# Kernel optimization log

Hardware: AMD Instinct MI355X
Metric: run time of the kernel (lower is better)

Reference implementation:

```python
import jax, jax.numpy as jnp
import numpy as np

N = 8192        # nodes
F_IN = 512      # input feature dim
H1 = 256        # args.hidden1
H2 = 64         # args.hidden2
E = 262144      # edges (avg degree 32)


def setup_inputs() -> dict:
    key = jax.random.key(0)
    ks = jax.random.split(key, 7)
    x = jax.random.normal(ks[0], (N, F_IN), dtype=jnp.float32)
    adj_rows = jax.random.randint(ks[1], (E,), 0, N, dtype=jnp.int32)
    adj_cols = jax.random.randint(ks[2], (E,), 0, N, dtype=jnp.int32)
    adj_vals = jax.random.uniform(ks[3], (E,), dtype=jnp.float32)
    # Xavier-uniform init like reset_parameters()
    def xavier(k, fan_in, fan_out):
        lim = jnp.sqrt(6.0 / (fan_in + fan_out))
        return jax.random.uniform(k, (fan_in, fan_out), jnp.float32, -lim, lim)
    W1 = xavier(ks[4], F_IN, H1)
    W2 = xavier(ks[5], H1, H2)
    W3 = xavier(ks[6], H1, H2)
    return {"x": x, "adj_rows": adj_rows, "adj_cols": adj_cols,
            "adj_vals": adj_vals, "W1": W1, "W2": W2, "W3": W3}


def reference(x, adj_rows, adj_cols, adj_vals, W1, W2, W3):
    n = x.shape[0]

    def spmm(support):
        # sparse [N,N] @ dense [N,D]: gather neighbor rows, scale, scatter-add
        return jax.ops.segment_sum(adj_vals[:, None] * support[adj_cols],
                                   adj_rows, num_segments=n)

    # gc1: dropout(no-op, eval) -> x @ W1 -> SpMM -> relu
    h1 = jax.nn.relu(spmm(x @ W1))
    # gc2 / gc3: identity activation
    mu = spmm(h1 @ W2)
    logvar = spmm(h1 @ W3)
    z = mu  # eval-mode reparameterize returns mu
    # InnerProductDecoder with identity act (dropout no-op in eval)
    adj_recon = z @ z.T  # [N, N]
    return adj_recon, z, mu, logvar
```

## Files before the change

kernel.cpp:

```cpp
#include <hip/hip_runtime.h>
#include <hip/hip_bf16.h>

#define N_NODES 8192
#define F_INDIM 512
#define H1DIM   256
#define H2DIM   64

typedef __bf16 bf16x8 __attribute__((ext_vector_type(8)));
typedef __bf16 bf16x4 __attribute__((ext_vector_type(4)));
typedef __bf16 bf16x2 __attribute__((ext_vector_type(2)));
typedef float  floatx4 __attribute__((ext_vector_type(4)));

__global__ void count_rows(const int* __restrict__ rows, int* __restrict__ cnt, int e) {
    int i = blockIdx.x * blockDim.x + threadIdx.x;
    if (i < e) atomicAdd(&cnt[rows[i]], 1);
}

__global__ void scan_rows(const int* __restrict__ cnt, int* __restrict__ row_ptr,
                          int* __restrict__ cursor, int n) {
    __shared__ int sums[1024];
    int t = threadIdx.x;
    int base = t * 8;
    int loc[8];
    int s = 0;
#pragma unroll
    for (int i = 0; i < 8; ++i) { loc[i] = cnt[base + i]; s += loc[i]; }
    sums[t] = s;
    __syncthreads();
    for (int off = 1; off < 1024; off <<= 1) {
        int v = (t >= off) ? sums[t - off] : 0;
        __syncthreads();
        sums[t] += v;
        __syncthreads();
    }
    int run = sums[t] - s;
#pragma unroll
    for (int i = 0; i < 8; ++i) {
        row_ptr[base + i] = run;
        cursor[base + i]  = run;
        run += loc[i];
    }
    if (t == 1023) row_ptr[n] = run;
}

__global__ void scatter_edges(const int* __restrict__ rows, const int* __restrict__ cols,
                              const float* __restrict__ vals, int* __restrict__ cursor,
                              int* __restrict__ csr_col, float* __restrict__ csr_val, int e) {
    int i = blockIdx.x * blockDim.x + threadIdx.x;
    if (i < e) {
        int r = rows[i];
        int slot = atomicAdd(&cursor[r], 1);
        csr_col[slot] = cols[i];
        csr_val[slot] = vals[i];
    }
}

__global__ void transpose_cast_w(const float* __restrict__ W1, const float* __restrict__ W2,
                                 const float* __restrict__ W3,
                                 __bf16* __restrict__ w1th, __bf16* __restrict__ w1tl,
                                 __bf16* __restrict__ w23th, __bf16* __restrict__ w23tl) {
    const int z = blockIdx.z;
    const float* src; __bf16 *oh, *ol; int K, N, rowoff, outld;
    if (z == 0)      { src = W1; K = 512; N = 256; oh = w1th;  ol = w1tl;  rowoff = 0;  outld = 512; }
    else if (z == 1) { src = W2; K = 256; N = 64;  oh = w23th; ol = w23tl; rowoff = 0;  outld = 256; }
    else             { src = W3; K = 256; N = 64;  oh = w23th; ol = w23tl; rowoff = 64; outld = 256; }
    const int kt = blockIdx.x, nt = blockIdx.y;
    if (kt * 32 >= K || nt * 32 >= N) return;
    __shared__ float tile[32][33];
    const int tx = threadIdx.x, ty = threadIdx.y;
#pragma unroll
    for (int j = 0; j < 4; ++j)
        tile[ty + 8 * j][tx] = src[(size_t)(kt * 32 + ty + 8 * j) * N + nt * 32 + tx];
    __syncthreads();
#pragma unroll
    for (int j = 0; j < 4; ++j) {
        int n = nt * 32 + ty + 8 * j;
        int k = kt * 32 + tx;
        float v = tile[tx][ty + 8 * j];
        __bf16 h = (__bf16)v;
        oh[(size_t)(rowoff + n) * outld + k] = h;
        ol[(size_t)(rowoff + n) * outld + k] = (__bf16)(v - (float)h);
    }
}

__global__ __launch_bounds__(256) void gemm1_mfma(const float* __restrict__ x,
                                                  const __bf16* __restrict__ bth,
                                                  const __bf16* __restrict__ btl,
                                                  float* __restrict__ C) {
    constexpr int K = F_INDIM, NN = H1DIM, LDSW = 40;
    __shared__ __bf16 Ah[64 * LDSW], Al[64 * LDSW], Bh[64 * LDSW], Bl[64 * LDSW];
    const int tid = threadIdx.x;
    const int m0 = blockIdx.y * 64, n0 = blockIdx.x * 64;
    const int lane = tid & 63, wv = tid >> 6;
    const int wm = wv >> 1, wn = wv & 1;
    const int r16 = lane & 15, q = lane >> 4;
    const int sr = tid >> 2, sc = (tid & 3) * 8;
    floatx4 acc[2][2] = {};

    for (int k0 = 0; k0 < K; k0 += 32) {
        floatx4 xa0 = *(const floatx4*)&x[(size_t)(m0 + sr) * K + k0 + sc];
        floatx4 xa1 = *(const floatx4*)&x[(size_t)(m0 + sr) * K + k0 + sc + 4];
        bf16x8 vb  = *(const bf16x8*)&bth[(size_t)(n0 + sr) * K + k0 + sc];
        bf16x8 vb2 = *(const bf16x8*)&btl[(size_t)(n0 + sr) * K + k0 + sc];
        bf16x8 va, va2;
#pragma unroll
        for (int j = 0; j < 4; ++j) {
            __bf16 h0 = (__bf16)xa0[j];
            va[j] = h0; va2[j] = (__bf16)(xa0[j] - (float)h0);
            __bf16 h1 = (__bf16)xa1[j];
            va[4 + j] = h1; va2[4 + j] = (__bf16)(xa1[j] - (float)h1);
        }
        __syncthreads();
        *(bf16x8*)&Ah[sr * LDSW + sc] = va;
        *(bf16x8*)&Bh[sr * LDSW + sc] = vb;
        *(bf16x8*)&Al[sr * LDSW + sc] = va2;
        *(bf16x8*)&Bl[sr * LDSW + sc] = vb2;
        __syncthreads();
        bf16x8 ah[2], al[2], bh[2], bl[2];
#pragma unroll
        for (int mt = 0; mt < 2; ++mt) {
            ah[mt] = *(const bf16x8*)&Ah[(wm * 32 + mt * 16 + r16) * LDSW + q * 8];
            al[mt] = *(const bf16x8*)&Al[(wm * 32 + mt * 16 + r16) * LDSW + q * 8];
        }
#pragma unroll
        for (int nt = 0; nt < 2; ++nt) {
            bh[nt] = *(const bf16x8*)&Bh[(wn * 32 + nt * 16 + r16) * LDSW + q * 8];
            bl[nt] = *(const bf16x8*)&Bl[(wn * 32 + nt * 16 + r16) * LDSW + q * 8];
        }
#pragma unroll
        for (int mt = 0; mt < 2; ++mt)
#pragma unroll
            for (int nt = 0; nt < 2; ++nt) {
                acc[mt][nt] = __builtin_amdgcn_mfma_f32_16x16x32_bf16(ah[mt], bh[nt], acc[mt][nt], 0, 0, 0);
                acc[mt][nt] = __builtin_amdgcn_mfma_f32_16x16x32_bf16(ah[mt], bl[nt], acc[mt][nt], 0, 0, 0);
                acc[mt][nt] = __builtin_amdgcn_mfma_f32_16x16x32_bf16(al[mt], bh[nt], acc[mt][nt], 0, 0, 0);
            }
    }
#pragma unroll
    for (int mt = 0; mt < 2; ++mt)
#pragma unroll
        for (int nt = 0; nt < 2; ++nt)
#pragma unroll
            for (int i = 0; i < 4; ++i) {
                int row = m0 + wm * 32 + mt * 16 + q * 4 + i;
                int col = n0 + wn * 32 + nt * 16 + r16;
                C[(size_t)row * NN + col] = acc[mt][nt][i];
            }
}

__global__ __launch_bounds__(256) void spmm_h1(const int* __restrict__ row_ptr,
                                               const int* __restrict__ csr_col,
                                               const float* __restrict__ csr_val,
                                               const float* __restrict__ in,
                                               __bf16* __restrict__ h1h,
                                               __bf16* __restrict__ h1l) {
    __shared__ int   s_col[4][64];
    __shared__ float s_val[4][64];
    const int tid = threadIdx.x;
    const int w = tid >> 6, lane = tid & 63;
    const int r = blockIdx.x * 4 + w;
    const int beg = row_ptr[r];
    const int deg = row_ptr[r + 1] - beg;
    const floatx4* in4 = (const floatx4*)in;
    floatx4 acc = {0.f, 0.f, 0.f, 0.f};
    for (int base = 0; base < deg; base += 64) {
        int m = deg - base; if (m > 64) m = 64;
        if (lane < m) {
            s_col[w][lane] = csr_col[beg + base + lane];
            s_val[w][lane] = csr_val[beg + base + lane];
        }
        int e = 0;
        for (; e + 4 <= m; e += 4) {
            int c0 = s_col[w][e],     c1 = s_col[w][e + 1];
            int c2 = s_col[w][e + 2], c3 = s_col[w][e + 3];
            float v0 = s_val[w][e],     v1 = s_val[w][e + 1];
            float v2 = s_val[w][e + 2], v3 = s_val[w][e + 3];
            floatx4 x0 = in4[(size_t)c0 * 64 + lane];
            floatx4 x1 = in4[(size_t)c1 * 64 + lane];
            floatx4 x2 = in4[(size_t)c2 * 64 + lane];
            floatx4 x3 = in4[(size_t)c3 * 64 + lane];
            acc += v0 * x0; acc += v1 * x1; acc += v2 * x2; acc += v3 * x3;
        }
        for (; e < m; ++e)
            acc += s_val[w][e] * in4[(size_t)s_col[w][e] * 64 + lane];
    }
    bf16x4 h, l;
#pragma unroll
    for (int j = 0; j < 4; ++j) {
        float rv = fmaxf(acc[j], 0.f);
        __bf16 hv = (__bf16)rv;
        h[j] = hv;
        l[j] = (__bf16)(rv - (float)hv);
    }
    *(bf16x4*)&h1h[(size_t)r * H1DIM + lane * 4] = h;
    *(bf16x4*)&h1l[(size_t)r * H1DIM + lane * 4] = l;
}

__global__ __launch_bounds__(256) void gemm23_mfma(const __bf16* __restrict__ ag_h,
                                                   const __bf16* __restrict__ ag_l,
                                                   const __bf16* __restrict__ bth,
                                                   const __bf16* __restrict__ btl,
                                                   float* __restrict__ t23) {
    constexpr int K = H1DIM, LDSW = 40;
    __shared__ __bf16 Ah[32 * LDSW], Al[32 * LDSW], Bh[128 * LDSW], Bl[128 * LDSW];
    const int tid = threadIdx.x;
    const int m0 = blockIdx.x * 32;
    const int lane = tid & 63, wn = tid >> 6;
    const int r16 = lane & 15, q = lane >> 4;
    const int ta = tid & 127;
    const int ar = ta >> 2, ac = (ta & 3) * 8;
    floatx4 acc[2][2] = {};

    for (int k0 = 0; k0 < K; k0 += 32) {
        const __bf16* asrc = (tid < 128) ? ag_h : ag_l;
        bf16x8 va = *(const bf16x8*)&asrc[(size_t)(m0 + ar) * K + k0 + ac];
        bf16x8 vbh[2], vbl[2];
#pragma unroll
        for (int v = 0; v < 2; ++v) {
            int id = tid + v * 256;
            int br = id >> 2, bc = (id & 3) * 8;
            vbh[v] = *(const bf16x8*)&bth[(size_t)br * K + k0 + bc];
            vbl[v] = *(const bf16x8*)&btl[(size_t)br * K + k0 + bc];
        }
        __syncthreads();
        {
            __bf16* adst = (tid < 128) ? Ah : Al;
            *(bf16x8*)&adst[ar * LDSW + ac] = va;
        }
#pragma unroll
        for (int v = 0; v < 2; ++v) {
            int id = tid + v * 256;
            int br = id >> 2, bc = (id & 3) * 8;
            *(bf16x8*)&Bh[br * LDSW + bc] = vbh[v];
            *(bf16x8*)&Bl[br * LDSW + bc] = vbl[v];
        }
        __syncthreads();
        bf16x8 ah[2], al[2], bh[2], bl[2];
#pragma unroll
        for (int mt = 0; mt < 2; ++mt) {
            ah[mt] = *(const bf16x8*)&Ah[(mt * 16 + r16) * LDSW + q * 8];
            al[mt] = *(const bf16x8*)&Al[(mt * 16 + r16) * LDSW + q * 8];
        }
#pragma unroll
        for (int nt = 0; nt < 2; ++nt) {
            bh[nt] = *(const bf16x8*)&Bh[(wn * 32 + nt * 16 + r16) * LDSW + q * 8];
            bl[nt] = *(const bf16x8*)&Bl[(wn * 32 + nt * 16 + r16) * LDSW + q * 8];
        }
#pragma unroll
        for (int mt = 0; mt < 2; ++mt)
#pragma unroll
            for (int nt = 0; nt < 2; ++nt) {
                acc[mt][nt] = __builtin_amdgcn_mfma_f32_16x16x32_bf16(ah[mt], bh[nt], acc[mt][nt], 0, 0, 0);
                acc[mt][nt] = __builtin_amdgcn_mfma_f32_16x16x32_bf16(ah[mt], bl[nt], acc[mt][nt], 0, 0, 0);
                acc[mt][nt] = __builtin_amdgcn_mfma_f32_16x16x32_bf16(al[mt], bh[nt], acc[mt][nt], 0, 0, 0);
            }
    }
#pragma unroll
    for (int mt = 0; mt < 2; ++mt)
#pragma unroll
        for (int nt = 0; nt < 2; ++nt)
#pragma unroll
            for (int i = 0; i < 4; ++i) {
                int row = m0 + mt * 16 + q * 4 + i;
                int col = wn * 32 + nt * 16 + r16;
                t23[(size_t)row * 128 + col] = acc[mt][nt][i];
            }
}

__global__ __launch_bounds__(256) void spmm_mu_logvar(const int* __restrict__ row_ptr,
                                                      const int* __restrict__ csr_col,
                                                      const float* __restrict__ csr_val,
                                                      const float* __restrict__ t23,
                                                      float* __restrict__ mu,
                                                      float* __restrict__ z,
                                                      float* __restrict__ logvar,
                                                      __bf16* __restrict__ zb) {
    __shared__ int   s_col[4][64];
    __shared__ float s_val[4][64];
    const int tid = threadIdx.x;
    const int w = tid >> 6, lane = tid & 63;
    const int r = blockIdx.x * 4 + w;
    const int beg = row_ptr[r];
    const int deg = row_ptr[r + 1] - beg;
    const float2* in2 = (const float2*)t23;
    float ax = 0.f, ay = 0.f;
    for (int base = 0; base < deg; base += 64) {
        int m = deg - base; if (m > 64) m = 64;
        if (lane < m) {
            s_col[w][lane] = csr_col[beg + base + lane];
            s_val[w][lane] = csr_val[beg + base + lane];
        }
        int e = 0;
        for (; e + 4 <= m; e += 4) {
            int c0 = s_col[w][e],     c1 = s_col[w][e + 1];
            int c2 = s_col[w][e + 2], c3 = s_col[w][e + 3];
            float v0 = s_val[w][e],     v1 = s_val[w][e + 1];
            float v2 = s_val[w][e + 2], v3 = s_val[w][e + 3];
            float2 x0 = in2[(size_t)c0 * 64 + lane];
            float2 x1 = in2[(size_t)c1 * 64 + lane];
            float2 x2 = in2[(size_t)c2 * 64 + lane];
            float2 x3 = in2[(size_t)c3 * 64 + lane];
            ax += v0 * x0.x + v1 * x1.x + v2 * x2.x + v3 * x3.x;
            ay += v0 * x0.y + v1 * x1.y + v2 * x2.y + v3 * x3.y;
        }
        for (; e < m; ++e) {
            float2 xv = in2[(size_t)s_col[w][e] * 64 + lane];
            float v = s_val[w][e];
            ax += v * xv.x;
            ay += v * xv.y;
        }
    }
    if (lane < 32) {
        size_t o2 = (size_t)r * 32 + lane;
        float2 v = {ax, ay};
        ((float2*)mu)[o2] = v;
        ((float2*)z)[o2] = v;
        bf16x2 b = {(__bf16)ax, (__bf16)ay};
        *(bf16x2*)&zb[(size_t)r * H2DIM + lane * 2] = b;
    } else {
        size_t o2 = (size_t)r * 32 + (lane - 32);
        float2 v = {ax, ay};
        ((float2*)logvar)[o2] = v;
    }
}

__global__ __launch_bounds__(256) void zzt_mfma(const __bf16* __restrict__ z,
                                                float* __restrict__ C) {
    constexpr int LDT = 132;
    __shared__ float tile[128 * LDT];
    const int tid = threadIdx.x;
    const int lane = tid & 63;
    const int wave = tid >> 6;
    const int wm = wave >> 1, wn = wave & 1;
    const int bm = blockIdx.y * 128, bn = blockIdx.x * 128;
    const int m0 = bm + wm * 64;
    const int n0 = bn + wn * 64;
    const int r16 = lane & 15;
    const int quad = lane >> 4;

    floatx4 acc[4][4] = {};
    const char* zc = (const char*)z;

#pragma unroll
    for (int h = 0; h < 2; ++h) {
        bf16x8 a[4], b[4];
#pragma unroll
        for (int mt = 0; mt < 4; ++mt)
            a[mt] = *(const bf16x8*)(zc + (m0 + mt * 16 + r16) * 128 + h * 64 + quad * 16);
#pragma unroll
        for (int nt = 0; nt < 4; ++nt)
            b[nt] = *(const bf16x8*)(zc + (n0 + nt * 16 + r16) * 128 + h * 64 + quad * 16);
#pragma unroll
        for (int mt = 0; mt < 4; ++mt)
#pragma unroll
            for (int nt = 0; nt < 4; ++nt)
                acc[mt][nt] = __builtin_amdgcn_mfma_f32_16x16x32_bf16(a[mt], b[nt], acc[mt][nt], 0, 0, 0);
    }

#pragma unroll
    for (int mt = 0; mt < 4; ++mt)
#pragma unroll
        for (int nt = 0; nt < 4; ++nt)
#pragma unroll
            for (int rr = 0; rr < 4; ++rr)
                tile[(wm * 64 + mt * 16 + quad * 4 + rr) * LDT + wn * 64 + nt * 16 + r16] =
                    acc[mt][nt][rr];
    __syncthreads();

    for (int i = tid; i < 128 * 32; i += 256) {
        int rr = i >> 5, cc = (i & 31) * 4;
        floatx4 v = *(const floatx4*)&tile[rr * LDT + cc];
        *(floatx4*)&C[(size_t)(bm + rr) * N_NODES + bn + cc] = v;
    }
}

extern "C" void kernel_launch(void* const* d_in, const int* in_sizes, int n_in,
                              void* d_out, int out_size, void* d_ws, size_t ws_size,
                              hipStream_t stream) {
    const float* x        = (const float*)d_in[0];
    const int*   adj_rows = (const int*)d_in[1];
    const int*   adj_cols = (const int*)d_in[2];
    const float* adj_vals = (const float*)d_in[3];
    const float* W1       = (const float*)d_in[4];
    const float* W2       = (const float*)d_in[5];
    const float* W3       = (const float*)d_in[6];
    const int E = in_sizes[1];
    const int n = N_NODES;

    char* ws = (char*)d_ws;
    size_t off = 0;
    auto alloc = [&](size_t bytes) {
        void* p = ws + off;
        off = (off + bytes + 255) & ~(size_t)255;
        return p;
    };
    int*    cnt     = (int*)alloc((size_t)n * 4);
    int*    row_ptr = (int*)alloc((size_t)(n + 1) * 4);
    int*    cursor  = (int*)alloc((size_t)n * 4);
    int*    csr_col = (int*)alloc((size_t)E * 4);
    float*  csr_val = (float*)alloc((size_t)E * 4);
    __bf16* w1th    = (__bf16*)alloc((size_t)H1DIM * F_INDIM * 2);
    __bf16* w1tl    = (__bf16*)alloc((size_t)H1DIM * F_INDIM * 2);
    __bf16* w23th   = (__bf16*)alloc((size_t)(2 * H2DIM) * H1DIM * 2);
    __bf16* w23tl   = (__bf16*)alloc((size_t)(2 * H2DIM) * H1DIM * 2);
    float*  support = (float*)alloc((size_t)n * H1DIM * 4);
    __bf16* h1h     = (__bf16*)alloc((size_t)n * H1DIM * 2);
    __bf16* h1l     = (__bf16*)alloc((size_t)n * H1DIM * 2);
    float*  t23     = (float*)alloc((size_t)n * 2 * H2DIM * 4);
    __bf16* zb      = (__bf16*)alloc((size_t)n * H2DIM * 2);

    float* out        = (float*)d_out;
    float* adj_recon  = out;
    float* z_out      = out + (size_t)n * n;
    float* mu_out     = z_out + (size_t)n * H2DIM;
    float* logvar_out = mu_out + (size_t)n * H2DIM;

    hipMemsetAsync(cnt, 0, (size_t)n * 4, stream);
    count_rows<<<(E + 255) / 256, 256, 0, stream>>>(adj_rows, cnt, E);
    scan_rows<<<1, 1024, 0, stream>>>(cnt, row_ptr, cursor, n);
    scatter_edges<<<(E + 255) / 256, 256, 0, stream>>>(adj_rows, adj_cols, adj_vals,
                                                       cursor, csr_col, csr_val, E);

    transpose_cast_w<<<dim3(16, 8, 3), dim3(32, 8), 0, stream>>>(W1, W2, W3,
                                                                 w1th, w1tl, w23th, w23tl);

    gemm1_mfma<<<dim3(H1DIM / 64, n / 64), 256, 0, stream>>>(x, w1th, w1tl, support);
    spmm_h1<<<n / 4, 256, 0, stream>>>(row_ptr, csr_col, csr_val, support, h1h, h1l);

    gemm23_mfma<<<n / 32, 256, 0, stream>>>(h1h, h1l, w23th, w23tl, t23);
    spmm_mu_logvar<<<n / 4, 256, 0, stream>>>(row_ptr, csr_col, csr_val, t23,
                                              mu_out, z_out, logvar_out, zb);

    zzt_mfma<<<dim3(n / 128, n / 128), 256, 0, stream>>>(zb, adj_recon);
}
```

Measured before the change: 405.2 us.

## Fuse first SpMM with the mu/logvar GEMM and use nontemporal output stores

```diff
diff --git a/kernel.cpp b/kernel.cpp
--- a/kernel.cpp
+++ b/kernel.cpp
@@ -10,6 +10,7 @@
 typedef __bf16 bf16x4 __attribute__((ext_vector_type(4)));
 typedef __bf16 bf16x2 __attribute__((ext_vector_type(2)));
 typedef float  floatx4 __attribute__((ext_vector_type(4)));
+typedef float  floatx2 __attribute__((ext_vector_type(2)));
 
 __global__ void count_rows(const int* __restrict__ rows, int* __restrict__ cnt, int e) {
     int i = blockIdx.x * blockDim.x + threadIdx.x;
@@ -148,123 +149,93 @@
             }
 }
 
-__global__ __launch_bounds__(256) void spmm_h1(const int* __restrict__ row_ptr,
-                                               const int* __restrict__ csr_col,
-                                               const float* __restrict__ csr_val,
-                                               const float* __restrict__ in,
-                                               __bf16* __restrict__ h1h,
-                                               __bf16* __restrict__ h1l) {
-    __shared__ int   s_col[4][64];
-    __shared__ float s_val[4][64];
-    const int tid = threadIdx.x;
-    const int w = tid >> 6, lane = tid & 63;
-    const int r = blockIdx.x * 4 + w;
-    const int beg = row_ptr[r];
-    const int deg = row_ptr[r + 1] - beg;
-    const floatx4* in4 = (const floatx4*)in;
-    floatx4 acc = {0.f, 0.f, 0.f, 0.f};
-    for (int base = 0; base < deg; base += 64) {
-        int m = deg - base; if (m > 64) m = 64;
-        if (lane < m) {
-            s_col[w][lane] = csr_col[beg + base + lane];
-            s_val[w][lane] = csr_val[beg + base + lane];
-        }
-        int e = 0;
-        for (; e + 4 <= m; e += 4) {
-            int c0 = s_col[w][e],     c1 = s_col[w][e + 1];
-            int c2 = s_col[w][e + 2], c3 = s_col[w][e + 3];
-            float v0 = s_val[w][e],     v1 = s_val[w][e + 1];
-            float v2 = s_val[w][e + 2], v3 = s_val[w][e + 3];
-            floatx4 x0 = in4[(size_t)c0 * 64 + lane];
-            floatx4 x1 = in4[(size_t)c1 * 64 + lane];
-            floatx4 x2 = in4[(size_t)c2 * 64 + lane];
-            floatx4 x3 = in4[(size_t)c3 * 64 + lane];
-            acc += v0 * x0; acc += v1 * x1; acc += v2 * x2; acc += v3 * x3;
-        }
-        for (; e < m; ++e)
-            acc += s_val[w][e] * in4[(size_t)s_col[w][e] * 64 + lane];
-    }
-    bf16x4 h, l;
-#pragma unroll
-    for (int j = 0; j < 4; ++j) {
-        float rv = fmaxf(acc[j], 0.f);
-        __bf16 hv = (__bf16)rv;
-        h[j] = hv;
-        l[j] = (__bf16)(rv - (float)hv);
-    }
-    *(bf16x4*)&h1h[(size_t)r * H1DIM + lane * 4] = h;
-    *(bf16x4*)&h1l[(size_t)r * H1DIM + lane * 4] = l;
-}
-
-__global__ __launch_bounds__(256) void gemm23_mfma(const __bf16* __restrict__ ag_h,
-                                                   const __bf16* __restrict__ ag_l,
+__global__ __launch_bounds__(512) void spmm_gemm23(const int* __restrict__ row_ptr,
+                                                   const int* __restrict__ csr_col,
+                                                   const float* __restrict__ csr_val,
+                                                   const float* __restrict__ support,
                                                    const __bf16* __restrict__ bth,
                                                    const __bf16* __restrict__ btl,
                                                    float* __restrict__ t23) {
-    constexpr int K = H1DIM, LDSW = 40;
-    __shared__ __bf16 Ah[32 * LDSW], Al[32 * LDSW], Bh[128 * LDSW], Bl[128 * LDSW];
+    constexpr int LDA = 264;
+    constexpr int LDSW = 40;
+    __shared__ __bf16 Ah[16 * LDA], Al[16 * LDA];
+    __shared__ __bf16 Bh[128 * LDSW], Bl[128 * LDSW];
+    __shared__ int   s_col[8][64];
+    __shared__ float s_val[8][64];
     const int tid = threadIdx.x;
-    const int m0 = blockIdx.x * 32;
-    const int lane = tid & 63, wn = tid >> 6;
+    const int w = tid >> 6, lane = tid & 63;
+    const int m0 = blockIdx.x * 16;
+
+    const float2* in2 = (const float2*)support;
+#pragma unroll
+    for (int p = 0; p < 2; ++p) {
+        const int coff = p * 64;
+#pragma unroll
+        for (int ri = 0; ri < 2; ++ri) {
+            const int rl = w * 2 + ri;
+            const int r = m0 + rl;
+            const int beg = row_ptr[r];
+            const int deg = row_ptr[r + 1] - beg;
+            float ax = 0.f, ay = 0.f;
+            for (int base = 0; base < deg; base += 64) {
+                int m = deg - base; if (m > 64) m = 64;
+                if (lane < m) {
+                    s_col[w][lane] = csr_col[beg + base + lane];
+                    s_val[w][lane] = csr_val[beg + base + lane];
+                }
+                int e = 0;
+                for (; e + 4 <= m; e += 4) {
+                    int c0 = s_col[w][e],     c1 = s_col[w][e + 1];
+                    int c2 = s_col[w][e + 2], c3 = s_col[w][e + 3];
+                    float v0 = s_val[w][e],     v1 = s_val[w][e + 1];
+                    float v2 = s_val[w][e + 2], v3 = s_val[w][e + 3];
+                    float2 x0 = in2[(size_t)c0 * 128 + coff + lane];
+                    float2 x1 = in2[(size_t)c1 * 128 + coff + lane];
+                    float2 x2 = in2[(size_t)c2 * 128 + coff + lane];
+                    float2 x3 = in2[(size_t)c3 * 128 + coff + lane];
+                    ax += v0 * x0.x + v1 * x1.x + v2 * x2.x + v3 * x3.x;
+                    ay += v0 * x0.y + v1 * x1.y + v2 * x2.y + v3 * x3.y;
+                }
+                for (; e < m; ++e) {
+                    float2 xv = in2[(size_t)s_col[w][e] * 128 + coff + lane];
+                    float v = s_val[w][e];
+                    ax += v * xv.x;
+                    ay += v * xv.y;
+                }
+            }
+            float rx = fmaxf(ax, 0.f), ry = fmaxf(ay, 0.f);
+            __bf16 hx = (__bf16)rx, hy = (__bf16)ry;
+            bf16x2 hv = {hx, hy};
+            bf16x2 lv = {(__bf16)(rx - (float)hx), (__bf16)(ry - (float)hy)};
+            const int kb = p * 128 + lane * 2;
+            *(bf16x2*)&Ah[rl * LDA + kb] = hv;
+            *(bf16x2*)&Al[rl * LDA + kb] = lv;
+        }
+    }
     const int r16 = lane & 15, q = lane >> 4;
-    const int ta = tid & 127;
-    const int ar = ta >> 2, ac = (ta & 3) * 8;
-    floatx4 acc[2][2] = {};
-
-    for (int k0 = 0; k0 < K; k0 += 32) {
-        const __bf16* asrc = (tid < 128) ? ag_h : ag_l;
-        bf16x8 va = *(const bf16x8*)&asrc[(size_t)(m0 + ar) * K + k0 + ac];
-        bf16x8 vbh[2], vbl[2];
-#pragma unroll
-        for (int v = 0; v < 2; ++v) {
-            int id = tid + v * 256;
-            int br = id >> 2, bc = (id & 3) * 8;
-            vbh[v] = *(const bf16x8*)&bth[(size_t)br * K + k0 + bc];
-            vbl[v] = *(const bf16x8*)&btl[(size_t)br * K + k0 + bc];
-        }
-        __syncthreads();
-        {
-            __bf16* adst = (tid < 128) ? Ah : Al;
-            *(bf16x8*)&adst[ar * LDSW + ac] = va;
-        }
-#pragma unroll
-        for (int v = 0; v < 2; ++v) {
-            int id = tid + v * 256;
-            int br = id >> 2, bc = (id & 3) * 8;
-            *(bf16x8*)&Bh[br * LDSW + bc] = vbh[v];
-            *(bf16x8*)&Bl[br * LDSW + bc] = vbl[v];
-        }
-        __syncthreads();
-        bf16x8 ah[2], al[2], bh[2], bl[2];
-#pragma unroll
-        for (int mt = 0; mt < 2; ++mt) {
-            ah[mt] = *(const bf16x8*)&Ah[(mt * 16 + r16) * LDSW + q * 8];
-            al[mt] = *(const bf16x8*)&Al[(mt * 16 + r16) * LDSW + q * 8];
-        }
-#pragma unroll
-        for (int nt = 0; nt < 2; ++nt) {
-            bh[nt] = *(const bf16x8*)&Bh[(wn * 32 + nt * 16 + r16) * LDSW + q * 8];
-            bl[nt] = *(const bf16x8*)&Bl[(wn * 32 + nt * 16 + r16) * LDSW + q * 8];
-        }
-#pragma unroll
-        for (int mt = 0; mt < 2; ++mt)
-#pragma unroll
-            for (int nt = 0; nt < 2; ++nt) {
-                acc[mt][nt] = __builtin_amdgcn_mfma_f32_16x16x32_bf16(ah[mt], bh[nt], acc[mt][nt], 0, 0, 0);
-                acc[mt][nt] = __builtin_amdgcn_mfma_f32_16x16x32_bf16(ah[mt], bl[nt], acc[mt][nt], 0, 0, 0);
-                acc[mt][nt] = __builtin_amdgcn_mfma_f32_16x16x32_bf16(al[mt], bh[nt], acc[mt][nt], 0, 0, 0);
-            }
-    }
-#pragma unroll
-    for (int mt = 0; mt < 2; ++mt)
-#pragma unroll
-        for (int nt = 0; nt < 2; ++nt)
-#pragma unroll
-            for (int i = 0; i < 4; ++i) {
-                int row = m0 + mt * 16 + q * 4 + i;
-                int col = wn * 32 + nt * 16 + r16;
-                t23[(size_t)row * 128 + col] = acc[mt][nt][i];
-            }
+    const int br = tid >> 2, bc = (tid & 3) * 8;
+    floatx4 acc = {};
+    for (int k0 = 0; k0 < H1DIM; k0 += 32) {
+        bf16x8 vbh = *(const bf16x8*)&bth[(size_t)br * H1DIM + k0 + bc];
+        bf16x8 vbl = *(const bf16x8*)&btl[(size_t)br * H1DIM + k0 + bc];
+        __syncthreads();
+        *(bf16x8*)&Bh[br * LDSW + bc] = vbh;
+        *(bf16x8*)&Bl[br * LDSW + bc] = vbl;
+        __syncthreads();
+        bf16x8 ah = *(const bf16x8*)&Ah[r16 * LDA + k0 + q * 8];
+        bf16x8 al = *(const bf16x8*)&Al[r16 * LDA + k0 + q * 8];
+        bf16x8 bh = *(const bf16x8*)&Bh[(w * 16 + r16) * LDSW + q * 8];
+        bf16x8 bl = *(const bf16x8*)&Bl[(w * 16 + r16) * LDSW + q * 8];
+        acc = __builtin_amdgcn_mfma_f32_16x16x32_bf16(ah, bh, acc, 0, 0, 0);
+        acc = __builtin_amdgcn_mfma_f32_16x16x32_bf16(ah, bl, acc, 0, 0, 0);
+        acc = __builtin_amdgcn_mfma_f32_16x16x32_bf16(al, bh, acc, 0, 0, 0);
+    }
+#pragma unroll
+    for (int i = 0; i < 4; ++i) {
+        int row = m0 + q * 4 + i;
+        int col = w * 16 + r16;
+        t23[(size_t)row * 128 + col] = acc[i];
+    }
 }
 
 __global__ __launch_bounds__(256) void spmm_mu_logvar(const int* __restrict__ row_ptr,
@@ -310,17 +281,16 @@
             ay += v * xv.y;
         }
     }
+    floatx2 v = {ax, ay};
     if (lane < 32) {
         size_t o2 = (size_t)r * 32 + lane;
-        float2 v = {ax, ay};
-        ((float2*)mu)[o2] = v;
-        ((float2*)z)[o2] = v;
+        __builtin_nontemporal_store(v, (floatx2*)mu + o2);
+        __builtin_nontemporal_store(v, (floatx2*)z + o2);
         bf16x2 b = {(__bf16)ax, (__bf16)ay};
         *(bf16x2*)&zb[(size_t)r * H2DIM + lane * 2] = b;
     } else {
         size_t o2 = (size_t)r * 32 + (lane - 32);
-        float2 v = {ax, ay};
-        ((float2*)logvar)[o2] = v;
+        __builtin_nontemporal_store(v, (floatx2*)logvar + o2);
     }
 }
 
@@ -370,7 +340,7 @@
     for (int i = tid; i < 128 * 32; i += 256) {
         int rr = i >> 5, cc = (i & 31) * 4;
         floatx4 v = *(const floatx4*)&tile[rr * LDT + cc];
-        *(floatx4*)&C[(size_t)(bm + rr) * N_NODES + bn + cc] = v;
+        __builtin_nontemporal_store(v, (floatx4*)&C[(size_t)(bm + rr) * N_NODES + bn + cc]);
     }
 }
 
@@ -404,8 +374,6 @@
     __bf16* w23th   = (__bf16*)alloc((size_t)(2 * H2DIM) * H1DIM * 2);
     __bf16* w23tl   = (__bf16*)alloc((size_t)(2 * H2DIM) * H1DIM * 2);
     float*  support = (float*)alloc((size_t)n * H1DIM * 4);
-    __bf16* h1h     = (__bf16*)alloc((size_t)n * H1DIM * 2);
-    __bf16* h1l     = (__bf16*)alloc((size_t)n * H1DIM * 2);
     float*  t23     = (float*)alloc((size_t)n * 2 * H2DIM * 4);
     __bf16* zb      = (__bf16*)alloc((size_t)n * H2DIM * 2);
 
@@ -425,9 +393,10 @@
                                                                  w1th, w1tl, w23th, w23tl);
 
     gemm1_mfma<<<dim3(H1DIM / 64, n / 64), 256, 0, stream>>>(x, w1th, w1tl, support);
-    spmm_h1<<<n / 4, 256, 0, stream>>>(row_ptr, csr_col, csr_val, support, h1h, h1l);
-
-    gemm23_mfma<<<n / 32, 256, 0, stream>>>(h1h, h1l, w23th, w23tl, t23);
+
+    spmm_gemm23<<<n / 16, 512, 0, stream>>>(row_ptr, csr_col, csr_val, support,
+                                            w23th, w23tl, t23);
+
     spmm_mu_logvar<<<n / 4, 256, 0, stream>>>(row_ptr, csr_col, csr_val, t23,
                                               mu_out, z_out, logvar_out, zb);
 
```

Result: faster. 397.0 us (-2.0%).
